# Kernel tuning notes

Measured on AMD Instinct MI355X. Metric: run time of the kernel, lower is better.

The kernel has to match this reference:

```python
import jax, jax.numpy as jnp
import numpy as np


def _apply_rope(x, cos, sin):
    # x: (..., T, D) with D even; cos/sin: (T, D), only even columns are used.
    x1, x2 = x[..., ::2], x[..., 1::2]
    c, s = cos[..., ::2], sin[..., ::2]
    even = x1 * c - x2 * s
    odd = x1 * s + x2 * c
    return jnp.stack((even, odd), axis=-1).reshape(x.shape)


def setup_inputs() -> dict:
    key = jax.random.key(0)
    B, T, C, H, G = 2, 2048, 4096, 32, 4  # batch, seq, n_embd, n_head, n_query_groups
    Dh = C // H            # 128
    n_kv = H // G          # 8 kv heads
    ks = jax.random.split(key, 5)
    w = 0.02
    x = jax.random.normal(ks[0], (B, T, C), jnp.float32)
    wq = jax.random.normal(ks[1], (C, H * Dh), jnp.float32) * w
    wk = jax.random.normal(ks[2], (C, n_kv * Dh), jnp.float32) * w
    wv = jax.random.normal(ks[3], (C, n_kv * Dh), jnp.float32) * w
    wo = jax.random.normal(ks[4], (C, C), jnp.float32) * w
    inv_freq = 1.0 / (10000.0 ** (jnp.arange(0, Dh, 2, dtype=jnp.float32) / Dh))
    ang = jnp.arange(T, dtype=jnp.float32)[:, None] * inv_freq[None, :]  # (T, Dh/2)
    cos = jnp.repeat(jnp.cos(ang), 2, axis=-1)  # (T, Dh)
    sin = jnp.repeat(jnp.sin(ang), 2, axis=-1)
    return {"x": x, "wq": wq, "wk": wk, "wv": wv, "wo": wo, "cos": cos, "sin": sin, "is_causal": 1}


def reference(x, wq, wk, wv, wo, cos, sin, is_causal):
    B, T, C = x.shape
    Dh = cos.shape[-1]
    H = wq.shape[1] // Dh
    n_kv = wk.shape[1] // Dh
    G = H // n_kv  # query-group repeat factor
    scale = 1.0 / jnp.sqrt(jnp.float32(Dh))

    q = (x @ wq).reshape(B, T, H, Dh).transpose(0, 2, 1, 3)      # (B,H,T,Dh)
    k = (x @ wk).reshape(B, T, n_kv, Dh).transpose(0, 2, 1, 3)   # (B,nkv,T,Dh)
    v = (x @ wv).reshape(B, T, n_kv, Dh).transpose(0, 2, 1, 3)

    c, s = cos[:T], sin[:T]
    q = _apply_rope(q, c, s)
    k = _apply_rope(k, c, s)

    # GQA without materializing repeated K/V: q head h attends kv head h // G
    # (matches repeat_interleave ordering: kv head j duplicated to q heads j*G..j*G+G-1)
    qg = q.reshape(B, n_kv, G, T, Dh)
    scores = jnp.einsum("bkgtd,bksd->bkgts", qg, k) * scale       # (B,nkv,G,T,T)
    if is_causal:
        mask = jnp.tril(jnp.ones((T, T), dtype=bool))
        scores = jnp.where(mask, scores, jnp.finfo(scores.dtype).min)
    attn = jax.nn.softmax(scores, axis=-1)
    out = jnp.einsum("bkgts,bksd->bkgtd", attn, v)                # (B,nkv,G,T,Dh)
    out = out.reshape(B, H, T, Dh).transpose(0, 2, 1, 3).reshape(B, T, C)
    return out @ wo
```

## Files before the change

### kernel.cpp

```cpp
#include <hip/hip_runtime.h>
#include <hip/hip_bf16.h>

#define BSZ   2
#define TSEQ  2048
#define CDIM  4096
#define NH    32
#define NKV   8
#define GQ    4
#define DH    128
#define BT    (BSZ * TSEQ)

typedef short   bf16x8  __attribute__((ext_vector_type(8)));
typedef float   f32x4   __attribute__((ext_vector_type(4)));
typedef unsigned short ushort8v __attribute__((ext_vector_type(8)));
typedef unsigned short u16;

#define LDS_AS(p) ((__attribute__((address_space(3))) void*)(p))
#define GLB_AS(p) ((const __attribute__((address_space(1))) void*)(p))

static __device__ inline unsigned short bf16_bits(float f) {
  __hip_bfloat16 h = __float2bfloat16(f);
  return *(unsigned short*)&h;
}
static __device__ inline float bits_f32(unsigned short u) {
  unsigned v = ((unsigned)u) << 16;
  return __builtin_bit_cast(float, v);
}

__global__ __launch_bounds__(256) void cvt_bf16x4(
    const float* __restrict__ src, __hip_bfloat16* __restrict__ dst, int n4) {
  int i = blockIdx.x * 256 + threadIdx.x;
  if (i >= n4) return;
  float4 v = ((const float4*)src)[i];
  ushort4 o;
  o.x = bf16_bits(v.x); o.y = bf16_bits(v.y);
  o.z = bf16_bits(v.z); o.w = bf16_bits(v.w);
  ((ushort4*)dst)[i] = o;
}

__global__ __launch_bounds__(256) void transpose_cvt(
    const float* __restrict__ src, __hip_bfloat16* __restrict__ dst, int K, int N) {
  __shared__ float T[64][65];
  const int bn = blockIdx.x * 64;
  const int bk = blockIdx.y * 64;
  const int tid = threadIdx.x;
  for (int i = tid; i < 64 * 16; i += 256) {
    int r = i >> 4, c4 = i & 15;
    float4 v = *(const float4*)&src[(size_t)(bk + r) * N + bn + c4 * 4];
    T[r][c4*4+0] = v.x; T[r][c4*4+1] = v.y; T[r][c4*4+2] = v.z; T[r][c4*4+3] = v.w;
  }
  __syncthreads();
  for (int i = tid; i < 64 * 16; i += 256) {
    int n = i >> 4, k4 = i & 15;
    ushort4 o;
    o.x = bf16_bits(T[k4*4+0][n]); o.y = bf16_bits(T[k4*4+1][n]);
    o.z = bf16_bits(T[k4*4+2][n]); o.w = bf16_bits(T[k4*4+3][n]);
    *(ushort4*)&dst[(size_t)(bn + n) * K + bk + k4 * 4] = o;
  }
}

__global__ __launch_bounds__(256) void gemm_mfma(
    const __hip_bfloat16* __restrict__ A, const __hip_bfloat16* __restrict__ Bt,
    void* __restrict__ C, int N, int K, int outBf16) {
  __shared__ __hip_bfloat16 As[128 * 32];
  __shared__ __hip_bfloat16 Bs[128 * 32];
  const int tid  = threadIdx.x;
  const int lane = tid & 63;
  const int wv   = tid >> 6;
  const int row0 = blockIdx.y * 128;
  const int col0 = blockIdx.x * 128;
  const int wm   = (wv & 1) * 64;
  const int wn   = (wv >> 1) * 64;
  const int lrow = lane & 15;
  const int kgrp = lane >> 4;

  f32x4 zero = {0.f, 0.f, 0.f, 0.f};
  f32x4 acc[4][4];
  #pragma unroll
  for (int mi = 0; mi < 4; ++mi)
    #pragma unroll
    for (int ni = 0; ni < 4; ++ni) acc[mi][ni] = zero;

  for (int k0 = 0; k0 < K; k0 += 32) {
    #pragma unroll
    for (int r = 0; r < 2; ++r) {
      int idx16 = r * 256 + tid;
      int arow  = idx16 >> 2;
      int akk   = (idx16 & 3) << 3;
      const __hip_bfloat16* ga = &A [(size_t)(row0 + arow) * K + k0 + akk];
      const __hip_bfloat16* gb = &Bt[(size_t)(col0 + arow) * K + k0 + akk];
      char* la = (char*)As + (r * 4096 + wv * 1024 + lane * 16);
      char* lb = (char*)Bs + (r * 4096 + wv * 1024 + lane * 16);
      __builtin_amdgcn_global_load_lds(GLB_AS(ga), LDS_AS(la), 16, 0, 0);
      __builtin_amdgcn_global_load_lds(GLB_AS(gb), LDS_AS(lb), 16, 0, 0);
    }
    __syncthreads();
    bf16x8 af[4], bfr[4];
    #pragma unroll
    for (int i = 0; i < 4; ++i) {
      af[i]  = *(const bf16x8*)&As[(wm + i * 16 + lrow) * 32 + kgrp * 8];
      bfr[i] = *(const bf16x8*)&Bs[(wn + i * 16 + lrow) * 32 + kgrp * 8];
    }
    #pragma unroll
    for (int mi = 0; mi < 4; ++mi)
      #pragma unroll
      for (int ni = 0; ni < 4; ++ni)
        acc[mi][ni] = __builtin_amdgcn_mfma_f32_16x16x32_bf16(af[mi], bfr[ni], acc[mi][ni], 0, 0, 0);
    __syncthreads();
  }

  if (outBf16) {
    __hip_bfloat16* Cb = (__hip_bfloat16*)C;
    #pragma unroll
    for (int mi = 0; mi < 4; ++mi)
      #pragma unroll
      for (int ni = 0; ni < 4; ++ni) {
        int col = col0 + wn + ni * 16 + lrow;
        int rowb = row0 + wm + mi * 16 + kgrp * 4;
        #pragma unroll
        for (int r = 0; r < 4; ++r)
          Cb[(size_t)(rowb + r) * N + col] = __float2bfloat16(acc[mi][ni][r]);
      }
  } else {
    float* Cf = (float*)C;
    #pragma unroll
    for (int mi = 0; mi < 4; ++mi)
      #pragma unroll
      for (int ni = 0; ni < 4; ++ni) {
        int col = col0 + wn + ni * 16 + lrow;
        int rowb = row0 + wm + mi * 16 + kgrp * 4;
        #pragma unroll
        for (int r = 0; r < 4; ++r)
          Cf[(size_t)(rowb + r) * N + col] = acc[mi][ni][r];
      }
  }
}

__global__ __launch_bounds__(512, 2) void gemm256(
    const __hip_bfloat16* __restrict__ A, const __hip_bfloat16* __restrict__ Bt,
    void* __restrict__ C, int N, int K, int outBf16) {
  __shared__ __hip_bfloat16 AsBuf[2][16384];
  __shared__ __hip_bfloat16 BsBuf[2][16384];

  const int tid  = threadIdx.x;
  const int lane = tid & 63;
  const int wid  = tid >> 6;
  const int wm   = wid >> 2;
  const int wn   = wid & 3;
  const int quad = lane >> 4;
  const int l15  = lane & 15;

  const int nbx = N >> 8;
  int bid = blockIdx.y * nbx + blockIdx.x;
  const int nwg = nbx * (int)gridDim.y;
  if ((nwg & 7) == 0) bid = (bid & 7) * (nwg >> 3) + (bid >> 3);
  const int row0 = (bid / nbx) << 8;
  const int col0 = (bid % nbx) << 8;

  const int NT = K >> 6;

  const int xr  = (l15 & 7) << 4;
  const int ke0 = (((quad * 16)      ^ xr) >> 1);
  const int ke1 = (((64 + quad * 16) ^ xr) >> 1);
  const int arE = (wm * 128 + l15) * 64;
  const int brE = (wn * 64  + l15) * 64;

#define STG(srcp, r0g, ldsb, h, k0e) do {                                          \
    _Pragma("unroll")                                                              \
    for (int j = 0; j < 2; ++j) {                                                  \
      int p    = (j * 512 + tid) << 4;                      \
      int prow = p >> 7;                                                           \
      int koff = (p & 127) ^ ((prow & 7) << 4);                                    \
      const __hip_bfloat16* gsrc =                                                 \
          (srcp) + (size_t)((r0g) + (h) * 128 + prow) * K + (k0e) + (koff >> 1);   \
      char* ldst = (char*)(ldsb) + (h) * 16384 + p;                                \
      __builtin_amdgcn_global_load_lds(GLB_AS(gsrc), LDS_AS(ldst), 16, 0, 0);      \
    }                                                                              \
  } while (0)

  f32x4 acc[8][4];
  #pragma unroll
  for (int i = 0; i < 8; ++i)
    #pragma unroll
    for (int j = 0; j < 4; ++j) acc[i][j] = (f32x4){0.f, 0.f, 0.f, 0.f};

  STG(A,  row0, &AsBuf[0][0], 0, 0);
  STG(A,  row0, &AsBuf[0][0], 1, 0);
  STG(Bt, col0, &BsBuf[0][0], 0, 0);
  STG(Bt, col0, &BsBuf[0][0], 1, 0);
  if (NT > 1) {
    STG(Bt, col0, &BsBuf[1][0], 0, 64);
    STG(Bt, col0, &BsBuf[1][0], 1, 64);
    asm volatile("s_waitcnt vmcnt(4)" ::: "memory");
  } else {
    asm volatile("s_waitcnt vmcnt(0)" ::: "memory");
  }
  __builtin_amdgcn_s_barrier();

  for (int t = 0; t < NT; ++t) {
    const int d  = t & 1, od = d ^ 1;
    char* Aod = (char*)&AsBuf[od][0];
    char* Bd  = (char*)&BsBuf[d][0];
    const int k1 = (t + 1) << 6, k2 = (t + 2) << 6;
    bf16x8 aH[4][2], b0[2][2], b1[2][2];

    #pragma unroll
    for (int m = 0; m < 4; ++m) {
      aH[m][0] = *(const bf16x8*)&AsBuf[d][arE + m * 1024 + ke0];
      aH[m][1] = *(const bf16x8*)&AsBuf[d][arE + m * 1024 + ke1];
    }
    #pragma unroll
    for (int n = 0; n < 2; ++n) {
      b0[n][0] = *(const bf16x8*)&BsBuf[d][brE + n * 1024 + ke0];
      b0[n][1] = *(const bf16x8*)&BsBuf[d][brE + n * 1024 + ke1];
    }
    if (t + 1 < NT) STG(A, row0, Aod, 0, k1);
    __builtin_amdgcn_s_barrier();
    asm volatile("s_waitcnt lgkmcnt(0)" ::: "memory");
    __builtin_amdgcn_s_setprio(1);
    #pragma unroll
    for (int m = 0; m < 4; ++m)
      #pragma unroll
      for (int n = 0; n < 2; ++n) {
        acc[m][n] = __builtin_amdgcn_mfma_f32_16x16x32_bf16(aH[m][0], b0[n][0], acc[m][n], 0, 0, 0);
        acc[m][n] = __builtin_amdgcn_mfma_f32_16x16x32_bf16(aH[m][1], b0[n][1], acc[m][n], 0, 0, 0);
      }
    __builtin_amdgcn_s_setprio(0);
    __builtin_amdgcn_s_barrier();

    #pragma unroll
    for (int n = 0; n < 2; ++n) {
      b1[n][0] = *(const bf16x8*)&BsBuf[d][brE + (n + 2) * 1024 + ke0];
      b1[n][1] = *(const bf16x8*)&BsBuf[d][brE + (n + 2) * 1024 + ke1];
    }
    if (t + 1 < NT) STG(A, row0, Aod, 1, k1);
    __builtin_amdgcn_s_barrier();
    asm volatile("s_waitcnt lgkmcnt(0)" ::: "memory");
    __builtin_amdgcn_s_setprio(1);
    #pragma unroll
    for (int m = 0; m < 4; ++m)
      #pragma unroll
      for (int n = 0; n < 2; ++n) {
        acc[m][n + 2] = __builtin_amdgcn_mfma_f32_16x16x32_bf16(aH[m][0], b1[n][0], acc[m][n + 2], 0, 0, 0);
        acc[m][n + 2] = __builtin_amdgcn_mfma_f32_16x16x32_bf16(aH[m][1], b1[n][1], acc[m][n + 2], 0, 0, 0);
      }
    __builtin_amdgcn_s_setprio(0);
    __builtin_amdgcn_s_barrier();

    #pragma unroll
    for (int m = 0; m < 4; ++m) {
      aH[m][0] = *(const bf16x8*)&AsBuf[d][arE + 4096 + m * 1024 + ke0];
      aH[m][1] = *(const bf16x8*)&AsBuf[d][arE + 4096 + m * 1024 + ke1];
    }
    if (t + 2 < NT) STG(Bt, col0, Bd, 0, k2);
    __builtin_amdgcn_s_barrier();
    asm volatile("s_waitcnt lgkmcnt(0)" ::: "memory");
    __builtin_amdgcn_s_setprio(1);
    #pragma unroll
    for (int m = 0; m < 4; ++m)
      #pragma unroll
      for (int n = 0; n < 2; ++n) {
        acc[m + 4][n + 2] = __builtin_amdgcn_mfma_f32_16x16x32_bf16(aH[m][0], b1[n][0], acc[m + 4][n + 2], 0, 0, 0);
        acc[m + 4][n + 2] = __builtin_amdgcn_mfma_f32_16x16x32_bf16(aH[m][1], b1[n][1], acc[m + 4][n + 2], 0, 0, 0);
      }
    __builtin_amdgcn_s_setprio(0);
    __builtin_amdgcn_s_barrier();

    if (t + 2 < NT) STG(Bt, col0, Bd, 1, k2);
    __builtin_amdgcn_s_barrier();
    __builtin_amdgcn_s_setprio(1);
    #pragma unroll
    for (int m = 0; m < 4; ++m)
      #pragma unroll
      for (int n = 0; n < 2; ++n) {
        acc[m + 4][n] = __builtin_amdgcn_mfma_f32_16x16x32_bf16(aH[m][0], b0[n][0], acc[m + 4][n], 0, 0, 0);
        acc[m + 4][n] = __builtin_amdgcn_mfma_f32_16x16x32_bf16(aH[m][1], b0[n][1], acc[m + 4][n], 0, 0, 0);
      }
    __builtin_amdgcn_s_setprio(0);
    if (t < NT - 2)       asm volatile("s_waitcnt vmcnt(4)" ::: "memory");
    else if (t == NT - 2) asm volatile("s_waitcnt vmcnt(0)" ::: "memory");
    __builtin_amdgcn_s_barrier();
  }
#undef STG

  if (outBf16) {
    __hip_bfloat16* Cb = (__hip_bfloat16*)C;
    #pragma unroll
    for (int mi = 0; mi < 8; ++mi)
      #pragma unroll
      for (int ni = 0; ni < 4; ++ni) {
        int col  = col0 + wn * 64 + ni * 16 + l15;
        int rowb = row0 + wm * 128 + mi * 16 + quad * 4;
        #pragma unroll
        for (int r = 0; r < 4; ++r)
          Cb[(size_t)(rowb + r) * N + col] = __float2bfloat16(acc[mi][ni][r]);
      }
  } else {
    float* Cf = (float*)C;
    #pragma unroll
    for (int mi = 0; mi < 8; ++mi)
      #pragma unroll
      for (int ni = 0; ni < 4; ++ni) {
        int col  = col0 + wn * 64 + ni * 16 + l15;
        int rowb = row0 + wm * 128 + mi * 16 + quad * 4;
        #pragma unroll
        for (int r = 0; r < 4; ++r)
          Cf[(size_t)(rowb + r) * N + col] = acc[mi][ni][r];
      }
  }
}

__global__ __launch_bounds__(256) void rope_bf16(
    __hip_bfloat16* __restrict__ buf, int stride, int perRow,
    const float* __restrict__ cosb, const float* __restrict__ sinb) {
  int idx = blockIdx.x * 256 + threadIdx.x;
  int row = idx / perRow;
  if (row >= BT) return;
  int c8 = (idx - row * perRow) * 8;
  int t  = row & (TSEQ - 1);
  int cp = c8 & (DH - 1);
  __hip_bfloat16* p = buf + (size_t)row * stride + c8;
  ushort8v raw = *(const ushort8v*)p;
  const float* cr = &cosb[(size_t)t * DH + cp];
  const float* sr = &sinb[(size_t)t * DH + cp];
  ushort8v outp;
  #pragma unroll
  for (int j = 0; j < 8; j += 2) {
    float x1 = bits_f32(raw[j]), x2 = bits_f32(raw[j + 1]);
    float c = cr[j], s = sr[j];
    outp[j]     = bf16_bits(x1 * c - x2 * s);
    outp[j + 1] = bf16_bits(x1 * s + x2 * c);
  }
  *(ushort8v*)p = outp;
}

__global__ __launch_bounds__(256) void transpose_v(
    const __hip_bfloat16* __restrict__ kvsrc, u16* __restrict__ vt) {
  __shared__ u16 T[64][72];
  const int tid  = threadIdx.x;
  const int tile = blockIdx.x, kvh = blockIdx.y, b = blockIdx.z;
  u16* dst = vt + ((size_t)((b * NKV + kvh) * 32 + tile)) * (128 * 64);
  for (int half = 0; half < 2; ++half) {
    #pragma unroll
    for (int it = 0; it < 2; ++it) {
      int idx = it * 256 + tid;
      int r = idx >> 3, c8 = idx & 7;
      ushort8v vdat = *(const ushort8v*)&kvsrc[
          (size_t)(b * TSEQ + tile * 64 + r) * 2048 + 1024 + kvh * DH + half * 64 + c8 * 8];
      *(ushort8v*)&T[r][c8 * 8] = vdat;
    }
    __syncthreads();
    #pragma unroll
    for (int it = 0; it < 2; ++it) {
      int idx = it * 256 + tid;
      int d = idx >> 3, c8 = idx & 7;
      ushort8v o8;
      #pragma unroll
      for (int j = 0; j < 8; ++j) o8[j] = T[c8 * 8 + j][d];
      *(ushort8v*)&dst[(size_t)(half * 64 + d) * 64 + c8 * 8] = o8;
    }
    __syncthreads();
  }
}

#define PSTR 68

__global__ __launch_bounds__(512, 4) void flash_mfma(
    const __hip_bfloat16* __restrict__ q,
    const __hip_bfloat16* __restrict__ kv,
    const u16* __restrict__ vt,
    __hip_bfloat16* __restrict__ o,
    const int* __restrict__ causal_p) {
  __shared__ u16 Ks[64 * 128];
  __shared__ u16 Vs[128 * 64];
  __shared__ u16 Ps[8][16 * PSTR];

  const int tid  = threadIdx.x;
  const int lane = tid & 63;
  const int wq   = tid >> 6;
  const int quad = lane >> 4;
  const int l15  = lane & 15;
  const int mtile = (int)gridDim.x - 1 - (int)blockIdx.x;
  const int h = blockIdx.y, b = blockIdx.z;
  const int kvh = h >> 2;
  const int m0  = mtile * 128;
  const bool causal = (*causal_p != 0);
  const float NEG_INF = -__builtin_inff();
  const float scale = 0.08838834764831845f;
  const int swz = (l15 & 7) << 3;
  const int qr0 = m0 + wq * 16 + quad * 4;
  const int qrMax = m0 + wq * 16 + 15;

  bf16x8 qf[4];
  {
    const __hip_bfloat16* qrow =
        &q[(size_t)(b * TSEQ + m0 + wq * 16 + l15) * CDIM + h * DH + quad * 8];
    #pragma unroll
    for (int kc = 0; kc < 4; ++kc) qf[kc] = *(const bf16x8*)(qrow + kc * 32);
  }

  f32x4 Ot[8];
  #pragma unroll
  for (int dt = 0; dt < 8; ++dt) Ot[dt] = (f32x4){0.f, 0.f, 0.f, 0.f};
  float mrow[4] = {NEG_INF, NEG_INF, NEG_INF, NEG_INF};
  float lrow[4] = {0.f, 0.f, 0.f, 0.f};

  const int ntiles = causal ? (2 * mtile + 2) : (TSEQ / 64);
  u16* Pw = &Ps[wq][0];
  const u16* vtbase = vt + ((size_t)(b * NKV + kvh) * 32) * (128 * 64);

  ushort8v kreg[2], vreg[2];
  #pragma unroll
  for (int it = 0; it < 2; ++it) {
    int idx = it * 512 + tid;
    int r = idx >> 4, c8 = idx & 15;
    kreg[it] = *(const ushort8v*)&kv[(size_t)(b * TSEQ + r) * 2048 + kvh * DH + c8 * 8];
    int d = idx >> 3, c8v = idx & 7;
    vreg[it] = *(const ushort8v*)&vtbase[(size_t)d * 64 + c8v * 8];
  }
  #pragma unroll
  for (int it = 0; it < 2; ++it) {
    int idx = it * 512 + tid;
    int r = idx >> 4, c8 = idx & 15;
    *(ushort8v*)&Ks[r * 128 + ((c8 ^ (r & 7)) * 8)] = kreg[it];
    int d = idx >> 3, c8v = idx & 7;
    *(ushort8v*)&Vs[d * 64 + ((c8v ^ (d & 7)) * 8)] = vreg[it];
  }
  __syncthreads();

  for (int tile = 0; tile < ntiles; ++tile) {
    const int j0 = tile * 64;
    if (tile + 1 < ntiles) {
      const u16* vblob = vtbase + (size_t)(tile + 1) * (128 * 64);
      #pragma unroll
      for (int it = 0; it < 2; ++it) {
        int idx = it * 512 + tid;
        int r = idx >> 4, c8 = idx & 15;
        kreg[it] = *(const ushort8v*)&kv[(size_t)(b * TSEQ + j0 + 64 + r) * 2048 + kvh * DH + c8 * 8];
        int d = idx >> 3, c8v = idx & 7;
        vreg[it] = *(const ushort8v*)&vblob[(size_t)d * 64 + c8v * 8];
      }
    }

    const bool active = !causal || (j0 <= qrMax);
    if (active) {
      f32x4 S[4];
      #pragma unroll
      for (int jt = 0; jt < 4; ++jt) {
        f32x4 acc = {0.f, 0.f, 0.f, 0.f};
        #pragma unroll
        for (int kc = 0; kc < 4; ++kc) {
          bf16x8 kf = *(const bf16x8*)&Ks[(jt * 16 + l15) * 128 + ((kc * 32 + quad * 8) ^ swz)];
          acc = __builtin_amdgcn_mfma_f32_16x16x32_bf16(qf[kc], kf, acc, 0, 0, 0);
        }
        S[jt] = acc;
      }
      #pragma unroll
      for (int jt = 0; jt < 4; ++jt)
        #pragma unroll
        for (int r = 0; r < 4; ++r) S[jt][r] *= scale;
      if (causal && (j0 + 63 > m0 + wq * 16)) {
        #pragma unroll
        for (int jt = 0; jt < 4; ++jt)
          #pragma unroll
          for (int r = 0; r < 4; ++r)
            if (j0 + jt * 16 + l15 > qr0 + r) S[jt][r] = NEG_INF;
      }

      float alpha[4], rsum[4];
      #pragma unroll
      for (int r = 0; r < 4; ++r) {
        float mx = fmaxf(fmaxf(S[0][r], S[1][r]), fmaxf(S[2][r], S[3][r]));
        #pragma unroll
        for (int w = 1; w <= 8; w <<= 1) mx = fmaxf(mx, __shfl_xor(mx, w));
        float mn = fmaxf(mrow[r], mx);
        alpha[r] = __expf(mrow[r] - mn);
        mrow[r] = mn;
        rsum[r] = 0.f;
      }
      #pragma unroll
      for (int jt = 0; jt < 4; ++jt)
        #pragma unroll
        for (int r = 0; r < 4; ++r) {
          float p = __expf(S[jt][r] - mrow[r]);
          rsum[r] += p;
          Pw[(quad * 4 + r) * PSTR + jt * 16 + l15] = bf16_bits(p);
        }
      #pragma unroll
      for (int r = 0; r < 4; ++r) {
        float s = rsum[r];
        #pragma unroll
        for (int w = 1; w <= 8; w <<= 1) s += __shfl_xor(s, w);
        lrow[r] = lrow[r] * alpha[r] + s;
      }
      #pragma unroll
      for (int dt = 0; dt < 8; ++dt)
        #pragma unroll
        for (int r = 0; r < 4; ++r) Ot[dt][r] *= alpha[r];

      #pragma unroll
      for (int kc = 0; kc < 2; ++kc) {
        bf16x8 pf = *(const bf16x8*)&Pw[l15 * PSTR + kc * 32 + quad * 8];
        #pragma unroll
        for (int dt = 0; dt < 8; ++dt) {
          bf16x8 vf = *(const bf16x8*)&Vs[(dt * 16 + l15) * 64 + ((kc * 32 + quad * 8) ^ swz)];
          Ot[dt] = __builtin_amdgcn_mfma_f32_16x16x32_bf16(pf, vf, Ot[dt], 0, 0, 0);
        }
      }
    }

    if (tile + 1 < ntiles) {
      __syncthreads();
      #pragma unroll
      for (int it = 0; it < 2; ++it) {
        int idx = it * 512 + tid;
        int r = idx >> 4, c8 = idx & 15;
        *(ushort8v*)&Ks[r * 128 + ((c8 ^ (r & 7)) * 8)] = kreg[it];
        int d = idx >> 3, c8v = idx & 7;
        *(ushort8v*)&Vs[d * 64 + ((c8v ^ (d & 7)) * 8)] = vreg[it];
      }
      __syncthreads();
    }
  }

  float invl[4];
  #pragma unroll
  for (int r = 0; r < 4; ++r) invl[r] = 1.f / lrow[r];
  #pragma unroll
  for (int dt = 0; dt < 8; ++dt)
    #pragma unroll
    for (int r = 0; r < 4; ++r)
      o[(size_t)(b * TSEQ + m0 + wq * 16 + quad * 4 + r) * CDIM + h * DH + dt * 16 + l15] =
          __float2bfloat16(Ot[dt][r] * invl[r]);
}

extern "C" void kernel_launch(void* const* d_in, const int* in_sizes, int n_in,
                              void* d_out, int out_size, void* d_ws, size_t ws_size,
                              hipStream_t stream) {
  const float* x    = (const float*)d_in[0];
  const float* wq   = (const float*)d_in[1];
  const float* wk   = (const float*)d_in[2];
  const float* wv   = (const float*)d_in[3];
  const float* wo   = (const float*)d_in[4];
  const float* cosb = (const float*)d_in[5];
  const float* sinb = (const float*)d_in[6];
  const int* causal = (const int*)d_in[7];

  char* wsb = (char*)d_ws;
  __hip_bfloat16* xb   = (__hip_bfloat16*)(wsb);
  __hip_bfloat16* woT  = (__hip_bfloat16*)(wsb);
  __hip_bfloat16* wqT  = (__hip_bfloat16*)(wsb + (((size_t)32) << 20));
  __hip_bfloat16* obuf = (__hip_bfloat16*)(wsb + (((size_t)32) << 20));
  __hip_bfloat16* wkvT = (__hip_bfloat16*)(wsb + (((size_t)64) << 20));
  u16*            vtb  = (u16*)           (wsb + (((size_t)64) << 20));
  __hip_bfloat16* kvb  = (__hip_bfloat16*)(wsb + (((size_t)80) << 20));
  __hip_bfloat16* qb   = (__hip_bfloat16*)d_out;

  dim3 blk(256);
  dim3 blk5(512);
  cvt_bf16x4<<<dim3((BT * CDIM / 4 + 255) / 256), blk, 0, stream>>>(x, xb, BT * CDIM / 4);
  transpose_cvt<<<dim3(CDIM / 64, CDIM / 64), blk, 0, stream>>>(wq, wqT, CDIM, CDIM);
  transpose_cvt<<<dim3(1024 / 64, CDIM / 64), blk, 0, stream>>>(wk, wkvT, CDIM, 1024);
  transpose_cvt<<<dim3(1024 / 64, CDIM / 64), blk, 0, stream>>>(wv, wkvT + (size_t)1024 * CDIM, CDIM, 1024);
  gemm256<<<dim3(CDIM / 256, BT / 256), blk5, 0, stream>>>(xb, wqT, qb, CDIM, CDIM, 1);
  gemm_mfma<<<dim3(2048 / 128, BT / 128), blk, 0, stream>>>(xb, wkvT, kvb, 2048, CDIM, 1);
  transpose_v<<<dim3(32, NKV, BSZ), blk, 0, stream>>>(kvb, vtb);
  rope_bf16<<<dim3(BT * (CDIM / 8) / 256), blk, 0, stream>>>(qb, CDIM, CDIM / 8, cosb, sinb);
  rope_bf16<<<dim3(BT * (1024 / 8) / 256), blk, 0, stream>>>(kvb, 2048, 1024 / 8, cosb, sinb);
  transpose_cvt<<<dim3(CDIM / 64, CDIM / 64), blk, 0, stream>>>(wo, woT, CDIM, CDIM);
  flash_mfma<<<dim3(TSEQ / 128, NH, BSZ), blk5, 0, stream>>>(qb, kvb, vtb, obuf, causal);
  gemm256<<<dim3(CDIM / 256, BT / 256), blk5, 0, stream>>>(obuf, woT, d_out, CDIM, CDIM, 0);
}
```

Before: 935.9 us.

## Process two query strips per flash block with lazy rescale and MFMA row sums

```diff
diff --git a/kernel.cpp b/kernel.cpp
--- a/kernel.cpp
+++ b/kernel.cpp
@@ -365,7 +365,73 @@
 
 #define PSTR 68
 
-__global__ __launch_bounds__(512, 4) void flash_mfma(
+#define STRIP_COMPUTE(QF, OT, OSUM, MROW, SB) do {                                  \
+    f32x4 S[4];                                                                     \
+    _Pragma("unroll")                                                               \
+    for (int jt = 0; jt < 4; ++jt) {                                                \
+      f32x4 acc4 = {0.f, 0.f, 0.f, 0.f};                                            \
+      _Pragma("unroll")                                                             \
+      for (int kc = 0; kc < 4; ++kc) {                                              \
+        bf16x8 kf = *(const bf16x8*)&Ks[(jt * 16 + l15) * 128 +                     \
+                                        ((kc * 32 + quad * 8) ^ swz)];              \
+        acc4 = __builtin_amdgcn_mfma_f32_16x16x32_bf16(QF[kc], kf, acc4, 0, 0, 0);  \
+      }                                                                             \
+      S[jt] = acc4;                                                                 \
+    }                                                                               \
+    _Pragma("unroll")                                                               \
+    for (int jt = 0; jt < 4; ++jt)                                                  \
+      _Pragma("unroll")                                                             \
+      for (int r = 0; r < 4; ++r) S[jt][r] *= scale;                                \
+    if (causal && (j0 + 63 > (SB))) {                                               \
+      _Pragma("unroll")                                                             \
+      for (int jt = 0; jt < 4; ++jt)                                                \
+        _Pragma("unroll")                                                           \
+        for (int r = 0; r < 4; ++r)                                                 \
+          if (j0 + jt * 16 + l15 > (SB) + quad * 4 + r) S[jt][r] = NEG_INF;         \
+    }                                                                               \
+    float pmax[4];                                                                  \
+    _Pragma("unroll")                                                               \
+    for (int r = 0; r < 4; ++r) {                                                   \
+      float mx = fmaxf(fmaxf(S[0][r], S[1][r]), fmaxf(S[2][r], S[3][r]));           \
+      _Pragma("unroll")                                                             \
+      for (int w = 1; w <= 8; w <<= 1) mx = fmaxf(mx, __shfl_xor(mx, w));           \
+      pmax[r] = mx;                                                                 \
+    }                                                                               \
+    bool need = false;                                                              \
+    _Pragma("unroll")                                                               \
+    for (int r = 0; r < 4; ++r) need = need || (pmax[r] > MROW[r] + 8.f);           \
+    if (__any(need ? 1 : 0)) {                                                      \
+      _Pragma("unroll")                                                             \
+      for (int r = 0; r < 4; ++r) {                                                 \
+        float mn = fmaxf(MROW[r], pmax[r]);                                         \
+        float al = __expf(MROW[r] - mn);                                            \
+        MROW[r] = mn;                                                               \
+        _Pragma("unroll")                                                           \
+        for (int dt = 0; dt < 8; ++dt) OT[dt][r] *= al;                             \
+        OSUM[r] *= al;                                                              \
+      }                                                                             \
+    }                                                                               \
+    _Pragma("unroll")                                                               \
+    for (int jt = 0; jt < 4; ++jt)                                                  \
+      _Pragma("unroll")                                                             \
+      for (int r = 0; r < 4; ++r) {                                                 \
+        float p = __expf(S[jt][r] - MROW[r]);                                       \
+        Pw[(quad * 4 + r) * PSTR + jt * 16 + l15] = bf16_bits(p);                   \
+      }                                                                             \
+    _Pragma("unroll")                                                               \
+    for (int kc = 0; kc < 2; ++kc) {                                                \
+      bf16x8 pf = *(const bf16x8*)&Pw[l15 * PSTR + kc * 32 + quad * 8];             \
+      OSUM = __builtin_amdgcn_mfma_f32_16x16x32_bf16(pf, onesf, OSUM, 0, 0, 0);     \
+      _Pragma("unroll")                                                             \
+      for (int dt = 0; dt < 8; ++dt) {                                              \
+        bf16x8 vf = *(const bf16x8*)&Vs[(dt * 16 + l15) * 64 +                      \
+                                        ((kc * 32 + quad * 8) ^ swz)];              \
+        OT[dt] = __builtin_amdgcn_mfma_f32_16x16x32_bf16(pf, vf, OT[dt], 0, 0, 0);  \
+      }                                                                             \
+    }                                                                               \
+  } while (0)
+
+__global__ __launch_bounds__(512, 3) void flash_mfma(
     const __hip_bfloat16* __restrict__ q,
     const __hip_bfloat16* __restrict__ kv,
     const u16* __restrict__ vt,
@@ -383,29 +449,41 @@
   const int mtile = (int)gridDim.x - 1 - (int)blockIdx.x;
   const int h = blockIdx.y, b = blockIdx.z;
   const int kvh = h >> 2;
-  const int m0  = mtile * 128;
+  const int m0  = mtile * 256;
   const bool causal = (*causal_p != 0);
   const float NEG_INF = -__builtin_inff();
   const float scale = 0.08838834764831845f;
   const int swz = (l15 & 7) << 3;
-  const int qr0 = m0 + wq * 16 + quad * 4;
-  const int qrMax = m0 + wq * 16 + 15;
-
-  bf16x8 qf[4];
+  const int sb0 = m0 + wq * 16;
+  const int sb1 = m0 + 128 + wq * 16;
+
+  bf16x8 qf0[4], qf1[4];
   {
-    const __hip_bfloat16* qrow =
-        &q[(size_t)(b * TSEQ + m0 + wq * 16 + l15) * CDIM + h * DH + quad * 8];
-    #pragma unroll
-    for (int kc = 0; kc < 4; ++kc) qf[kc] = *(const bf16x8*)(qrow + kc * 32);
-  }
-
-  f32x4 Ot[8];
-  #pragma unroll
-  for (int dt = 0; dt < 8; ++dt) Ot[dt] = (f32x4){0.f, 0.f, 0.f, 0.f};
-  float mrow[4] = {NEG_INF, NEG_INF, NEG_INF, NEG_INF};
-  float lrow[4] = {0.f, 0.f, 0.f, 0.f};
-
-  const int ntiles = causal ? (2 * mtile + 2) : (TSEQ / 64);
+    const __hip_bfloat16* qr0p =
+        &q[(size_t)(b * TSEQ + sb0 + l15) * CDIM + h * DH + quad * 8];
+    const __hip_bfloat16* qr1p =
+        &q[(size_t)(b * TSEQ + sb1 + l15) * CDIM + h * DH + quad * 8];
+    #pragma unroll
+    for (int kc = 0; kc < 4; ++kc) {
+      qf0[kc] = *(const bf16x8*)(qr0p + kc * 32);
+      qf1[kc] = *(const bf16x8*)(qr1p + kc * 32);
+    }
+  }
+  bf16x8 onesf;
+  #pragma unroll
+  for (int j = 0; j < 8; ++j) onesf[j] = (short)0x3F80;
+
+  f32x4 Ot0[8], Ot1[8];
+  #pragma unroll
+  for (int dt = 0; dt < 8; ++dt) {
+    Ot0[dt] = (f32x4){0.f, 0.f, 0.f, 0.f};
+    Ot1[dt] = (f32x4){0.f, 0.f, 0.f, 0.f};
+  }
+  f32x4 Osum0 = {0.f, 0.f, 0.f, 0.f}, Osum1 = {0.f, 0.f, 0.f, 0.f};
+  float mrow0[4] = {NEG_INF, NEG_INF, NEG_INF, NEG_INF};
+  float mrow1[4] = {NEG_INF, NEG_INF, NEG_INF, NEG_INF};
+
+  const int ntiles = causal ? (4 * mtile + 4) : (TSEQ / 64);
   u16* Pw = &Ps[wq][0];
   const u16* vtbase = vt + ((size_t)(b * NKV + kvh) * 32) * (128 * 64);
 
@@ -442,71 +520,11 @@
       }
     }
 
-    const bool active = !causal || (j0 <= qrMax);
-    if (active) {
-      f32x4 S[4];
-      #pragma unroll
-      for (int jt = 0; jt < 4; ++jt) {
-        f32x4 acc = {0.f, 0.f, 0.f, 0.f};
-        #pragma unroll
-        for (int kc = 0; kc < 4; ++kc) {
-          bf16x8 kf = *(const bf16x8*)&Ks[(jt * 16 + l15) * 128 + ((kc * 32 + quad * 8) ^ swz)];
-          acc = __builtin_amdgcn_mfma_f32_16x16x32_bf16(qf[kc], kf, acc, 0, 0, 0);
-        }
-        S[jt] = acc;
-      }
-      #pragma unroll
-      for (int jt = 0; jt < 4; ++jt)
-        #pragma unroll
-        for (int r = 0; r < 4; ++r) S[jt][r] *= scale;
-      if (causal && (j0 + 63 > m0 + wq * 16)) {
-        #pragma unroll
-        for (int jt = 0; jt < 4; ++jt)
-          #pragma unroll
-          for (int r = 0; r < 4; ++r)
-            if (j0 + jt * 16 + l15 > qr0 + r) S[jt][r] = NEG_INF;
-      }
-
-      float alpha[4], rsum[4];
-      #pragma unroll
-      for (int r = 0; r < 4; ++r) {
-        float mx = fmaxf(fmaxf(S[0][r], S[1][r]), fmaxf(S[2][r], S[3][r]));
-        #pragma unroll
-        for (int w = 1; w <= 8; w <<= 1) mx = fmaxf(mx, __shfl_xor(mx, w));
-        float mn = fmaxf(mrow[r], mx);
-        alpha[r] = __expf(mrow[r] - mn);
-        mrow[r] = mn;
-        rsum[r] = 0.f;
-      }
-      #pragma unroll
-      for (int jt = 0; jt < 4; ++jt)
-        #pragma unroll
-        for (int r = 0; r < 4; ++r) {
-          float p = __expf(S[jt][r] - mrow[r]);
-          rsum[r] += p;
-          Pw[(quad * 4 + r) * PSTR + jt * 16 + l15] = bf16_bits(p);
-        }
-      #pragma unroll
-      for (int r = 0; r < 4; ++r) {
-        float s = rsum[r];
-        #pragma unroll
-        for (int w = 1; w <= 8; w <<= 1) s += __shfl_xor(s, w);
-        lrow[r] = lrow[r] * alpha[r] + s;
-      }
-      #pragma unroll
-      for (int dt = 0; dt < 8; ++dt)
-        #pragma unroll
-        for (int r = 0; r < 4; ++r) Ot[dt][r] *= alpha[r];
-
-      #pragma unroll
-      for (int kc = 0; kc < 2; ++kc) {
-        bf16x8 pf = *(const bf16x8*)&Pw[l15 * PSTR + kc * 32 + quad * 8];
-        #pragma unroll
-        for (int dt = 0; dt < 8; ++dt) {
-          bf16x8 vf = *(const bf16x8*)&Vs[(dt * 16 + l15) * 64 + ((kc * 32 + quad * 8) ^ swz)];
-          Ot[dt] = __builtin_amdgcn_mfma_f32_16x16x32_bf16(pf, vf, Ot[dt], 0, 0, 0);
-        }
-      }
+    if (!causal || (j0 <= sb0 + 15)) {
+      STRIP_COMPUTE(qf0, Ot0, Osum0, mrow0, sb0);
+    }
+    if (!causal || (j0 <= sb1 + 15)) {
+      STRIP_COMPUTE(qf1, Ot1, Osum1, mrow1, sb1);
     }
 
     if (tile + 1 < ntiles) {
@@ -523,15 +541,20 @@
     }
   }
 
-  float invl[4];
-  #pragma unroll
-  for (int r = 0; r < 4; ++r) invl[r] = 1.f / lrow[r];
-  #pragma unroll
-  for (int dt = 0; dt < 8; ++dt)
-    #pragma unroll
-    for (int r = 0; r < 4; ++r)
-      o[(size_t)(b * TSEQ + m0 + wq * 16 + quad * 4 + r) * CDIM + h * DH + dt * 16 + l15] =
-          __float2bfloat16(Ot[dt][r] * invl[r]);
+  {
+    float invl0[4], invl1[4];
+    #pragma unroll
+    for (int r = 0; r < 4; ++r) { invl0[r] = 1.f / Osum0[r]; invl1[r] = 1.f / Osum1[r]; }
+    #pragma unroll
+    for (int dt = 0; dt < 8; ++dt)
+      #pragma unroll
+      for (int r = 0; r < 4; ++r) {
+        o[(size_t)(b * TSEQ + sb0 + quad * 4 + r) * CDIM + h * DH + dt * 16 + l15] =
+            __float2bfloat16(Ot0[dt][r] * invl0[r]);
+        o[(size_t)(b * TSEQ + sb1 + quad * 4 + r) * CDIM + h * DH + dt * 16 + l15] =
+            __float2bfloat16(Ot1[dt][r] * invl1[r]);
+      }
+  }
 }
 
 extern "C" void kernel_launch(void* const* d_in, const int* in_sizes, int n_in,
@@ -568,6 +591,6 @@
   rope_bf16<<<dim3(BT * (CDIM / 8) / 256), blk, 0, stream>>>(qb, CDIM, CDIM / 8, cosb, sinb);
   rope_bf16<<<dim3(BT * (1024 / 8) / 256), blk, 0, stream>>>(kvb, 2048, 1024 / 8, cosb, sinb);
   transpose_cvt<<<dim3(CDIM / 64, CDIM / 64), blk, 0, stream>>>(wo, woT, CDIM, CDIM);
-  flash_mfma<<<dim3(TSEQ / 128, NH, BSZ), blk5, 0, stream>>>(qb, kvb, vtb, obuf, causal);
+  flash_mfma<<<dim3(TSEQ / 256, NH, BSZ), blk5, 0, stream>>>(qb, kvb, vtb, obuf, causal);
   gemm256<<<dim3(CDIM / 256, BT / 256), blk5, 0, stream>>>(obuf, woT, d_out, CDIM, CDIM, 0);
 }
```

Result: slower. 1.071 ms (+14.5%).
